# Kernel tuning notes

Measured on AMD Instinct MI355X. Metric: run time of the kernel, lower is better.

## Reference

```python
import jax, jax.numpy as jnp
import numpy as np

D_MODEL = 1024
NUM_HEADS = 16
HEAD_DIM = D_MODEL // NUM_HEADS
THETA = 10000.0


def _rope(x, cos, sin):
    # x: [B, H, S, hd]; cos/sin: [S, hd//2] (broadcast over B, H)
    x_even = x[..., 0::2]
    x_odd = x[..., 1::2]
    y_even = x_even * cos - x_odd * sin
    y_odd = x_even * sin + x_odd * cos
    # interleave back: stack on last dim then flatten
    y = jnp.stack((y_even, y_odd), axis=-1)
    return y.reshape(x.shape)


def setup_inputs() -> dict:
    key = jax.random.key(0)
    ks = jax.random.split(key, 5)
    B, S = 2, 2048
    x = jax.random.normal(ks[0], (B, S, D_MODEL), dtype=jnp.float32)
    scale = 1.0 / np.sqrt(D_MODEL)
    Wq = jax.random.normal(ks[1], (D_MODEL, D_MODEL), dtype=jnp.float32) * scale
    Wk = jax.random.normal(ks[2], (D_MODEL, D_MODEL), dtype=jnp.float32) * scale
    Wv = jax.random.normal(ks[3], (D_MODEL, D_MODEL), dtype=jnp.float32) * scale
    Wo = jax.random.normal(ks[4], (D_MODEL, D_MODEL), dtype=jnp.float32) * scale
    token_positions = jnp.arange(S, dtype=jnp.int64 if jax.config.jax_enable_x64 else jnp.int32)
    return {"x": x, "token_positions": token_positions, "Wq": Wq, "Wk": Wk, "Wv": Wv, "Wo": Wo}


def reference(x, token_positions, Wq, Wk, Wv, Wo):
    B, S, _ = x.shape
    # nn.Linear(d,d,bias=False): y = x @ W.T
    q = (x @ Wq.T).reshape(B, S, NUM_HEADS, HEAD_DIM).transpose(0, 2, 1, 3)
    k = (x @ Wk.T).reshape(B, S, NUM_HEADS, HEAD_DIM).transpose(0, 2, 1, 3)
    v = (x @ Wv.T).reshape(B, S, NUM_HEADS, HEAD_DIM).transpose(0, 2, 1, 3)

    # RoPE tables gathered at token_positions
    freqs = 1.0 / THETA ** (jnp.arange(0, HEAD_DIM, 2, dtype=jnp.float32) / HEAD_DIM)
    angles = token_positions.astype(jnp.float32)[:, None] * freqs[None, :]  # [S, hd//2]
    cos, sin = jnp.cos(angles), jnp.sin(angles)
    q = _rope(q, cos, sin)
    k = _rope(k, cos, sin)

    scores = jnp.einsum("bhqd,bhkd->bhqk", q, k) / np.sqrt(HEAD_DIM)
    causal = jnp.tril(jnp.ones((S, S), dtype=bool))
    scores = jnp.where(causal, scores, jnp.finfo(scores.dtype).min)
    attn = jax.nn.softmax(scores, axis=-1)
    out = jnp.einsum("bhqk,bhkd->bhqd", attn, v)  # [B,H,S,hd]
    out = out.transpose(0, 2, 1, 3).reshape(B, S, D_MODEL)
    return out @ Wo.T
```

## Files before the change

### kernel.cpp

```cpp
#include <hip/hip_runtime.h>

#define S_LEN 2048
#define NH 16
#define HD 64
#define DM 1024
#define MTOT 4096

#define QSCALE 0.18033688011112042f

typedef short bf16x8 __attribute__((ext_vector_type(8)));
typedef float f32x4 __attribute__((ext_vector_type(4)));
typedef unsigned short u16x8 __attribute__((ext_vector_type(8)));

__device__ __forceinline__ unsigned short f2bf(float f) {
  unsigned int u = __builtin_bit_cast(unsigned int, f);
  u += 0x7fffu + ((u >> 16) & 1u);
  return (unsigned short)(u >> 16);
}
__device__ __forceinline__ unsigned short f2bf_fast(float f) {
  unsigned int u = __builtin_bit_cast(unsigned int, f);
  return (unsigned short)((u + 0x8000u) >> 16);
}

__device__ __forceinline__ void async_copy16(const void* g, void* l) {
  __builtin_amdgcn_global_load_lds(
      (const __attribute__((address_space(1))) unsigned int*)g,
      (__attribute__((address_space(3))) unsigned int*)l, 16, 0, 0);
}

__global__ void cvt_bf16_kernel(const float* __restrict__ src,
                                unsigned short* __restrict__ dst, int n) {
  int i = (blockIdx.x * 256 + threadIdx.x) * 8;
  if (i >= n) return;
  const float4* s = (const float4*)(src + i);
  float4 v0 = s[0], v1 = s[1];
  u16x8 o;
  o[0] = f2bf(v0.x); o[1] = f2bf(v0.y); o[2] = f2bf(v0.z); o[3] = f2bf(v0.w);
  o[4] = f2bf(v1.x); o[5] = f2bf(v1.y); o[6] = f2bf(v1.z); o[7] = f2bf(v1.w);
  *(u16x8*)(dst + i) = o;
}

__global__ void cvt_w_kernel(const float* __restrict__ w0, const float* __restrict__ w1,
                             const float* __restrict__ w2, const float* __restrict__ w3,
                             unsigned short* __restrict__ dst) {
  int z = blockIdx.y;
  const float* src = (z == 0) ? w0 : (z == 1) ? w1 : (z == 2) ? w2 : w3;
  int i = (blockIdx.x * 256 + threadIdx.x) * 8;
  const float4* s = (const float4*)(src + i);
  float4 v0 = s[0], v1 = s[1];
  u16x8 o;
  o[0] = f2bf(v0.x); o[1] = f2bf(v0.y); o[2] = f2bf(v0.z); o[3] = f2bf(v0.w);
  o[4] = f2bf(v1.x); o[5] = f2bf(v1.y); o[6] = f2bf(v1.z); o[7] = f2bf(v1.w);
  *(u16x8*)(dst + (size_t)z * DM * DM + i) = o;
}

__global__ void sincos_tab_kernel(const int* __restrict__ pos, float2* __restrict__ tab) {
  int idx = blockIdx.x * 256 + threadIdx.x;
  int s = idx >> 5, i = idx & 31;
  float fr = expf(-(float)i * 0.28782313662425574f);
  float ang = (float)pos[s] * fr;
  float sn, cs;
  sincosf(ang, &sn, &cs);
  tab[idx] = make_float2(cs, sn);
}

__device__ __forceinline__ void gemm_core(const unsigned short* __restrict__ A,
                                          const unsigned short* __restrict__ Bt,
                                          int m0, int n0, int K,
                                          char* a_lds, char* b_lds,
                                          f32x4 (&acc)[4][4]) {
  const int tid = threadIdx.x;
  const int w = tid >> 6, l = tid & 63;
  const int wr = w >> 1, wc = w & 1;
  const int c = l & 15, g = l >> 4;

  const size_t rs = (size_t)K * 2;
  const int lr = l >> 3;
  const int jsw = ((l & 7) ^ lr) << 4;
  const char* srcA = (const char*)A + ((size_t)m0 + w * 8 + lr) * rs + jsw;
  const char* srcB = (const char*)Bt + ((size_t)n0 + w * 8 + lr) * rs + jsw;
  char* dstA = a_lds + w * 1024 + l * 16;
  char* dstB = b_lds + w * 1024 + l * 16;
  const int csw = (c & 7) << 4;
  const int nsteps = K / 64;

  auto stage = [&](int buf, int kt) {
    const int off = buf * 16384;
#pragma unroll
    for (int i = 0; i < 4; ++i) {
      async_copy16(srcA + (size_t)i * 32 * rs + kt * 128, dstA + off + i * 4096);
      async_copy16(srcB + (size_t)i * 32 * rs + kt * 128, dstB + off + i * 4096);
    }
  };

  stage(0, 0);
  asm volatile("s_waitcnt vmcnt(0)" ::: "memory");
  __syncthreads();
  int cur = 0;

  for (int kt = 0; kt < nsteps; ++kt) {
    if (kt + 1 < nsteps) stage(cur ^ 1, kt + 1);
    const char* al = a_lds + cur * 16384;
    const char* bl = b_lds + cur * 16384;
    __builtin_amdgcn_s_setprio(1);
#pragma unroll
    for (int kk = 0; kk < 2; ++kk) {
      bf16x8 af[4], bfv[4];
#pragma unroll
      for (int mi = 0; mi < 4; ++mi)
        af[mi] = *(const bf16x8*)(al + (wr * 64 + mi * 16 + c) * 128 + ((kk * 64 + g * 16) ^ csw));
#pragma unroll
      for (int ni = 0; ni < 4; ++ni)
        bfv[ni] = *(const bf16x8*)(bl + (wc * 64 + ni * 16 + c) * 128 + ((kk * 64 + g * 16) ^ csw));
#pragma unroll
      for (int mi = 0; mi < 4; ++mi)
#pragma unroll
        for (int ni = 0; ni < 4; ++ni)
          acc[mi][ni] = __builtin_amdgcn_mfma_f32_16x16x32_bf16(af[mi], bfv[ni], acc[mi][ni], 0, 0, 0);
    }
    __builtin_amdgcn_s_setprio(0);
    asm volatile("s_waitcnt vmcnt(0)" ::: "memory");
    __syncthreads();
    cur ^= 1;
  }
}

__global__ __launch_bounds__(256)
void gemm_qkv_kernel(const unsigned short* __restrict__ X,
                     const unsigned short* __restrict__ Wq,
                     const unsigned short* __restrict__ Wk,
                     const unsigned short* __restrict__ Wv,
                     const float2* __restrict__ tab,
                     unsigned short* __restrict__ Qb,
                     unsigned short* __restrict__ Kb,
                     unsigned short* __restrict__ Vt) {
  __shared__ char a_lds[2 * 16384];
  __shared__ char b_lds[2 * 16384];
  const int z = blockIdx.z;
  const unsigned short* Bt = (z == 0) ? Wq : (z == 1) ? Wk : Wv;
  const int m0 = blockIdx.x * 128, n0 = blockIdx.y * 128;

  f32x4 acc[4][4] = {};
  gemm_core(X, Bt, m0, n0, DM, a_lds, b_lds, acc);

  const int tid = threadIdx.x;
  const int w = tid >> 6, l = tid & 63;
  const int wr = w >> 1, wc = w & 1;
  const int c = l & 15, g = l >> 4;

  if (z == 2) {
#pragma unroll
    for (int mi = 0; mi < 4; ++mi)
#pragma unroll
      for (int ni = 0; ni < 4; ++ni)
#pragma unroll
        for (int r = 0; r < 4; ++r) {
          int row = m0 + wr * 64 + mi * 16 + 4 * g + r;
          int col = n0 + wc * 64 + ni * 16 + c;
          int b = row >> 11, s = row & 2047;
          int h = col >> 6, d = col & 63;
          Vt[((size_t)(b * NH + h) * HD + d) * S_LEN + s] = f2bf(acc[mi][ni][r]);
        }
  } else {
    unsigned short* QK = z ? Kb : Qb;
    const float oscale = z ? 1.0f : QSCALE;
#pragma unroll
    for (int mi = 0; mi < 4; ++mi)
#pragma unroll
      for (int ni = 0; ni < 4; ++ni) {
        int col = n0 + wc * 64 + ni * 16 + c;
        int fi = (col >> 1) & 31;
        float sgn = (col & 1) ? 1.0f : -1.0f;
#pragma unroll
        for (int r = 0; r < 4; ++r) {
          int row = m0 + wr * 64 + mi * 16 + 4 * g + r;
          int b = row >> 11, s = row & 2047;
          float v = acc[mi][ni][r];
          float p = __shfl_xor(v, 1);
          float2 csn = tab[(s << 5) | fi];
          float vr = (v * csn.x + sgn * p * csn.y) * oscale;
          int h = col >> 6, d = col & 63;
          QK[((size_t)(b * NH + h) * S_LEN + s) * HD + d] = f2bf(vr);
        }
      }
  }
}

__global__ __launch_bounds__(256)
void gemm_out_kernel(const unsigned short* __restrict__ A,
                     const unsigned short* __restrict__ Wo,
                     float* __restrict__ out) {
  __shared__ char a_lds[2 * 16384];
  __shared__ char b_lds[2 * 16384];
  const int m0 = blockIdx.x * 128, n0 = blockIdx.y * 128;
  f32x4 acc[4][4] = {};
  gemm_core(A, Wo, m0, n0, DM, a_lds, b_lds, acc);

  const int tid = threadIdx.x;
  const int w = tid >> 6, l = tid & 63;
  const int wr = w >> 1, wc = w & 1;
  const int c = l & 15, g = l >> 4;
#pragma unroll
  for (int mi = 0; mi < 4; ++mi)
#pragma unroll
    for (int ni = 0; ni < 4; ++ni)
#pragma unroll
      for (int r = 0; r < 4; ++r) {
        int row = m0 + wr * 64 + mi * 16 + 4 * g + r;
        int col = n0 + wc * 64 + ni * 16 + c;
        out[(size_t)row * DM + col] = acc[mi][ni][r];
      }
}

#define PART_STRIDE 4160
__global__ __launch_bounds__(256, 4)
void attn_kernel(const unsigned short* __restrict__ Q,
                 const unsigned short* __restrict__ Kb,
                 const unsigned short* __restrict__ Vt,
                 float* __restrict__ part) {
  __shared__ char kbuf[2][8192];
  __shared__ char vbuf[2][8192];
  __shared__ unsigned short p_lds[4][16 * 64];
  const int tid = threadIdx.x;
  const int w = tid >> 6, l = tid & 63;
  const int g = l >> 4, c = l & 15;

  const unsigned int id = blockIdx.x;
  const int bh = id & 31;
  const int p = (id >> 5) & 1;
  const int qblk = 31 - (id >> 6);
  const int q0 = qblk * 64;

  const size_t base = (size_t)bh * (S_LEN * HD);
  const char* Kc = (const char*)(Kb + base);
  const char* Vc = (const char*)(Vt + base);

  const int lr = l >> 3;
  const int jsw = ((l & 7) << 4) ^ (lr << 4);
  const int r0 = w * 8 + lr;
  const int r1 = (4 + w) * 8 + lr;
  const char* ksrc0 = Kc + r0 * 128 + jsw;
  const char* ksrc1 = Kc + r1 * 128 + jsw;
  const char* vsrc0 = Vc + r0 * 4096 + jsw;
  const char* vsrc1 = Vc + r1 * 4096 + jsw;

  bf16x8 qf0, qf1;
  {
    const unsigned short* qp = Q + base + (size_t)(q0 + w * 16 + c) * HD + g * 8;
    qf0 = *(const bf16x8*)qp;
    qf1 = *(const bf16x8*)(qp + 32);
  }
  f32x4 oacc[4] = {};
  float rsum[4] = {0.f, 0.f, 0.f, 0.f};
  unsigned short* pl = &p_lds[w][0];
  const int csw = (c & 7) << 4;

  auto stage = [&](int buf, int t) {
    char* kd = &kbuf[buf][w * 1024 + l * 16];
    char* vd = &vbuf[buf][w * 1024 + l * 16];
    size_t ko = (size_t)t * 8192;
    size_t vo = (size_t)t * 128;
    async_copy16(ksrc0 + ko, kd);
    async_copy16(ksrc1 + ko, kd + 4096);
    async_copy16(vsrc0 + vo, vd);
    async_copy16(vsrc1 + vo, vd + 4096);
  };

  stage(0, p);
  asm volatile("s_waitcnt vmcnt(0)" ::: "memory");
  __syncthreads();
  int cur = 0;

  for (int t = p; t <= qblk; t += 2) {
    if (t + 2 <= qblk) stage(cur ^ 1, t + 2);
    const char* kl = kbuf[cur];
    const char* vl = vbuf[cur];
    const int kv0 = t * 64;

    f32x4 sc[4] = {};
    __builtin_amdgcn_s_setprio(1);
#pragma unroll
    for (int nt = 0; nt < 4; ++nt) {
      bf16x8 k0 = *(const bf16x8*)(kl + (nt * 16 + c) * 128 + ((g * 16) ^ csw));
      bf16x8 k1 = *(const bf16x8*)(kl + (nt * 16 + c) * 128 + ((64 + g * 16) ^ csw));
      sc[nt] = __builtin_amdgcn_mfma_f32_16x16x32_bf16(qf0, k0, sc[nt], 0, 0, 0);
      sc[nt] = __builtin_amdgcn_mfma_f32_16x16x32_bf16(qf1, k1, sc[nt], 0, 0, 0);
    }
    __builtin_amdgcn_s_setprio(0);

    if (t == qblk) {
#pragma unroll
      for (int nt = 0; nt < 4; ++nt)
#pragma unroll
        for (int r = 0; r < 4; ++r) {
          int kvi = kv0 + nt * 16 + c;
          int qi = q0 + w * 16 + 4 * g + r;
          sc[nt][r] = exp2f((kvi > qi) ? -1e30f : sc[nt][r]);
        }
    } else {
#pragma unroll
      for (int nt = 0; nt < 4; ++nt)
#pragma unroll
        for (int r = 0; r < 4; ++r)
          sc[nt][r] = exp2f(sc[nt][r]);
    }
#pragma unroll
    for (int nt = 0; nt < 4; ++nt)
#pragma unroll
      for (int r = 0; r < 4; ++r) {
        float pv = sc[nt][r];
        rsum[r] += pv;
        int row = 4 * g + r, col = nt * 16 + c;
        int byte = row * 128 + ((col * 2) ^ ((row & 7) << 4));
        *(unsigned short*)((char*)pl + byte) = f2bf_fast(pv);
      }
    asm volatile("" ::: "memory");
    __builtin_amdgcn_s_setprio(1);
#pragma unroll
    for (int ks = 0; ks < 2; ++ks) {
      int pbyte = c * 128 + ((ks * 64 + g * 16) ^ csw);
      bf16x8 pf = *(const bf16x8*)((char*)pl + pbyte);
#pragma unroll
      for (int nt = 0; nt < 4; ++nt) {
        bf16x8 vf = *(const bf16x8*)(vl + (nt * 16 + c) * 128 + ((ks * 64 + g * 16) ^ csw));
        oacc[nt] = __builtin_amdgcn_mfma_f32_16x16x32_bf16(pf, vf, oacc[nt], 0, 0, 0);
      }
    }
    __builtin_amdgcn_s_setprio(0);
    asm volatile("" ::: "memory");

    asm volatile("s_waitcnt vmcnt(0)" ::: "memory");
    __syncthreads();
    cur ^= 1;
  }

#pragma unroll
  for (int r = 0; r < 4; ++r) {
    float s = rsum[r];
    s += __shfl_xor(s, 1);
    s += __shfl_xor(s, 2);
    s += __shfl_xor(s, 4);
    s += __shfl_xor(s, 8);
    rsum[r] = s;
  }
  float* pa = part + ((size_t)(bh * 32 + qblk) * 2 + p) * PART_STRIDE;
#pragma unroll
  for (int nt = 0; nt < 4; ++nt)
#pragma unroll
    for (int r = 0; r < 4; ++r) {
      int row = w * 16 + 4 * g + r;
      int col = nt * 16 + c;
      __builtin_nontemporal_store(oacc[nt][r], &pa[row * 64 + col]);
    }
  if (c == 0) {
#pragma unroll
    for (int r = 0; r < 4; ++r) {
      int row = w * 16 + 4 * g + r;
      __builtin_nontemporal_store(rsum[r], &pa[4096 + row]);
    }
  }
}

__global__ __launch_bounds__(256)
void combine_kernel(const float* __restrict__ part, unsigned short* __restrict__ Ob) {
  const int qblk = blockIdx.x & 31;
  const int bh = blockIdx.x >> 5;
  const int b = bh >> 4, h = bh & 15;
  const int tid = threadIdx.x;
  const int row = tid >> 2, colb = (tid & 3) * 16;

  const float* p0 = part + ((size_t)(bh * 32 + qblk) * 2 + 0) * PART_STRIDE;
  const float* p1 = p0 + PART_STRIDE;
  float s0 = __builtin_nontemporal_load(&p0[4096 + row]);
  float s1 = __builtin_nontemporal_load(&p1[4096 + row]);
  float inv = 1.0f / (s0 + s1);

  int token = qblk * 64 + row;
  unsigned short* dst = Ob + ((size_t)b * S_LEN + token) * DM + h * HD + colb;
  const f32x4* a0 = (const f32x4*)(p0 + row * 64 + colb);
  const f32x4* a1 = (const f32x4*)(p1 + row * 64 + colb);
  u16x8 o0, o1;
#pragma unroll
  for (int q = 0; q < 2; ++q) {
    f32x4 v0 = __builtin_nontemporal_load(&a0[2 * q]);
    f32x4 v1 = __builtin_nontemporal_load(&a1[2 * q]);
    f32x4 w0 = __builtin_nontemporal_load(&a0[2 * q + 1]);
    f32x4 w1 = __builtin_nontemporal_load(&a1[2 * q + 1]);
    u16x8& oo = q ? o1 : o0;
    oo[0] = f2bf((v0[0] + v1[0]) * inv);
    oo[1] = f2bf((v0[1] + v1[1]) * inv);
    oo[2] = f2bf((v0[2] + v1[2]) * inv);
    oo[3] = f2bf((v0[3] + v1[3]) * inv);
    oo[4] = f2bf((w0[0] + w1[0]) * inv);
    oo[5] = f2bf((w0[1] + w1[1]) * inv);
    oo[6] = f2bf((w0[2] + w1[2]) * inv);
    oo[7] = f2bf((w0[3] + w1[3]) * inv);
  }
  *(u16x8*)dst = o0;
  *(u16x8*)(dst + 8) = o1;
}

extern "C" void kernel_launch(void* const* d_in, const int* in_sizes, int n_in,
                              void* d_out, int out_size, void* d_ws, size_t ws_size,
                              hipStream_t stream) {
  const float* x = (const float*)d_in[0];
  const int* tpos = (const int*)d_in[1];
  const float* wq = (const float*)d_in[2];
  const float* wk = (const float*)d_in[3];
  const float* wv = (const float*)d_in[4];
  const float* wo = (const float*)d_in[5];
  float* out = (float*)d_out;

  char* ws = (char*)d_ws;
  unsigned short* xb = (unsigned short*)(ws);
  unsigned short* wqb = (unsigned short*)(ws + 8388608);
  unsigned short* wkb = wqb + DM * DM;
  unsigned short* wvb = wqb + 2 * DM * DM;
  unsigned short* wob = wqb + 3 * DM * DM;
  unsigned short* qb = (unsigned short*)(ws + 16777216);
  unsigned short* kb = (unsigned short*)(ws + 16777216 + 8388608);
  unsigned short* vt = (unsigned short*)(ws + 16777216 + 2 * 8388608);
  unsigned short* ab = (unsigned short*)(ws + 16777216 + 3 * 8388608);
  float2* tab = (float2*)(ws + 50331648);
  float* part = (float*)(ws + 50855936);

  cvt_bf16_kernel<<<2048, 256, 0, stream>>>(x, xb, MTOT * DM);
  cvt_w_kernel<<<dim3(512, 4), 256, 0, stream>>>(wq, wk, wv, wo, wqb);
  sincos_tab_kernel<<<256, 256, 0, stream>>>(tpos, tab);

  gemm_qkv_kernel<<<dim3(32, 8, 3), 256, 0, stream>>>(xb, wqb, wkb, wvb, tab, qb, kb, vt);
  attn_kernel<<<2048, 256, 0, stream>>>(qb, kb, vt, part);
  combine_kernel<<<1024, 256, 0, stream>>>(part, ab);
  gemm_out_kernel<<<dim3(32, 8), 256, 0, stream>>>(ab, wob, out);
}
```

Before: 132.9 us.

## Drop split-KV partials and combine kernel; balance causal q-blocks across grid

The attention kernel no longer splits each query block's KV range into two interleaved halves, so it no longer writes fp32 partial outputs and row sums for a separate combine kernel. Each block now walks all KV tiles with a single-step double buffer, normalizes by the row sum itself, and writes bf16 output directly. Query blocks are ordered in a zigzag pattern so that short and long causal blocks are spread across the grid. This removes one launch and the partial-buffer round trip through memory, but halves the grid to 1024 blocks and doubles the longest per-block KV loop, which can hurt occupancy and tail latency.

```diff
diff --git a/kernel.cpp b/kernel.cpp
--- a/kernel.cpp
+++ b/kernel.cpp
@@ -212,12 +212,11 @@
       }
 }
 
-#define PART_STRIDE 4160
 __global__ __launch_bounds__(256, 4)
 void attn_kernel(const unsigned short* __restrict__ Q,
                  const unsigned short* __restrict__ Kb,
                  const unsigned short* __restrict__ Vt,
-                 float* __restrict__ part) {
+                 unsigned short* __restrict__ Ob) {
   __shared__ char kbuf[2][8192];
   __shared__ char vbuf[2][8192];
   __shared__ unsigned short p_lds[4][16 * 64];
@@ -227,8 +226,9 @@
 
   const unsigned int id = blockIdx.x;
   const int bh = id & 31;
-  const int p = (id >> 5) & 1;
-  const int qblk = 31 - (id >> 6);
+  const int j = id >> 5;
+  const int a = j & 7, kk = j >> 3;
+  const int qblk = (kk == 0) ? a : (kk == 1) ? (15 - a) : (kk == 2) ? (16 + a) : (31 - a);
   const int q0 = qblk * 64;
 
   const size_t base = (size_t)bh * (S_LEN * HD);
@@ -266,13 +266,13 @@
     async_copy16(vsrc1 + vo, vd + 4096);
   };
 
-  stage(0, p);
+  stage(0, 0);
   asm volatile("s_waitcnt vmcnt(0)" ::: "memory");
   __syncthreads();
   int cur = 0;
 
-  for (int t = p; t <= qblk; t += 2) {
-    if (t + 2 <= qblk) stage(cur ^ 1, t + 2);
+  for (int t = 0; t <= qblk; ++t) {
+    if (t + 1 <= qblk) stage(cur ^ 1, t + 1);
     const char* kl = kbuf[cur];
     const char* vl = vbuf[cur];
     const int kv0 = t * 64;
@@ -341,63 +341,17 @@
     s += __shfl_xor(s, 2);
     s += __shfl_xor(s, 4);
     s += __shfl_xor(s, 8);
-    rsum[r] = s;
-  }
-  float* pa = part + ((size_t)(bh * 32 + qblk) * 2 + p) * PART_STRIDE;
+    rsum[r] = 1.0f / s;
+  }
+  const int b = bh >> 4, h = bh & 15;
 #pragma unroll
   for (int nt = 0; nt < 4; ++nt)
 #pragma unroll
     for (int r = 0; r < 4; ++r) {
-      int row = w * 16 + 4 * g + r;
+      int qi = q0 + w * 16 + 4 * g + r;
       int col = nt * 16 + c;
-      __builtin_nontemporal_store(oacc[nt][r], &pa[row * 64 + col]);
-    }
-  if (c == 0) {
-#pragma unroll
-    for (int r = 0; r < 4; ++r) {
-      int row = w * 16 + 4 * g + r;
-      __builtin_nontemporal_store(rsum[r], &pa[4096 + row]);
-    }
-  }
-}
-
-__global__ __launch_bounds__(256)
-void combine_kernel(const float* __restrict__ part, unsigned short* __restrict__ Ob) {
-  const int qblk = blockIdx.x & 31;
-  const int bh = blockIdx.x >> 5;
-  const int b = bh >> 4, h = bh & 15;
-  const int tid = threadIdx.x;
-  const int row = tid >> 2, colb = (tid & 3) * 16;
-
-  const float* p0 = part + ((size_t)(bh * 32 + qblk) * 2 + 0) * PART_STRIDE;
-  const float* p1 = p0 + PART_STRIDE;
-  float s0 = __builtin_nontemporal_load(&p0[4096 + row]);
-  float s1 = __builtin_nontemporal_load(&p1[4096 + row]);
-  float inv = 1.0f / (s0 + s1);
-
-  int token = qblk * 64 + row;
-  unsigned short* dst = Ob + ((size_t)b * S_LEN + token) * DM + h * HD + colb;
-  const f32x4* a0 = (const f32x4*)(p0 + row * 64 + colb);
-  const f32x4* a1 = (const f32x4*)(p1 + row * 64 + colb);
-  u16x8 o0, o1;
-#pragma unroll
-  for (int q = 0; q < 2; ++q) {
-    f32x4 v0 = __builtin_nontemporal_load(&a0[2 * q]);
-    f32x4 v1 = __builtin_nontemporal_load(&a1[2 * q]);
-    f32x4 w0 = __builtin_nontemporal_load(&a0[2 * q + 1]);
-    f32x4 w1 = __builtin_nontemporal_load(&a1[2 * q + 1]);
-    u16x8& oo = q ? o1 : o0;
-    oo[0] = f2bf((v0[0] + v1[0]) * inv);
-    oo[1] = f2bf((v0[1] + v1[1]) * inv);
-    oo[2] = f2bf((v0[2] + v1[2]) * inv);
-    oo[3] = f2bf((v0[3] + v1[3]) * inv);
-    oo[4] = f2bf((w0[0] + w1[0]) * inv);
-    oo[5] = f2bf((w0[1] + w1[1]) * inv);
-    oo[6] = f2bf((w0[2] + w1[2]) * inv);
-    oo[7] = f2bf((w0[3] + w1[3]) * inv);
-  }
-  *(u16x8*)dst = o0;
-  *(u16x8*)(dst + 8) = o1;
+      Ob[((size_t)b * S_LEN + qi) * DM + h * HD + col] = f2bf(oacc[nt][r] * rsum[r]);
+    }
 }
 
 extern "C" void kernel_launch(void* const* d_in, const int* in_sizes, int n_in,
@@ -422,14 +376,12 @@
   unsigned short* vt = (unsigned short*)(ws + 16777216 + 2 * 8388608);
   unsigned short* ab = (unsigned short*)(ws + 16777216 + 3 * 8388608);
   float2* tab = (float2*)(ws + 50331648);
-  float* part = (float*)(ws + 50855936);
 
   cvt_bf16_kernel<<<2048, 256, 0, stream>>>(x, xb, MTOT * DM);
   cvt_w_kernel<<<dim3(512, 4), 256, 0, stream>>>(wq, wk, wv, wo, wqb);
   sincos_tab_kernel<<<256, 256, 0, stream>>>(tpos, tab);
 
   gemm_qkv_kernel<<<dim3(32, 8, 3), 256, 0, stream>>>(xb, wqb, wkb, wvb, tab, qb, kb, vt);
-  attn_kernel<<<2048, 256, 0, stream>>>(qb, kb, vt, part);
-  combine_kernel<<<1024, 256, 0, stream>>>(part, ab);
+  attn_kernel<<<1024, 256, 0, stream>>>(qb, kb, vt, ab);
   gemm_out_kernel<<<dim3(32, 8), 256, 0, stream>>>(ab, wob, out);
 }
```

After: 126.4 us. -4.9%, faster.
